# Performance work log

Hardware: AMD Instinct MI355X
Metric: run time of the kernel (lower is better)

The kernel has to match this reference:

```python
import jax, jax.numpy as jnp
import numpy as np

K = 3    # kernel_size
PAD = 1  # floor(K/2) * padding_flag


def ste_sign(x):
    # Binarize to {-1, 0, +1} (torch.sign semantics) with straight-through
    # gradient (identity), matching BNN training where grads flow to weight.org.
    return x + jax.lax.stop_gradient(jnp.sign(x) - x)


def setup_inputs() -> dict:
    key = jax.random.key(0)
    k1, k2 = jax.random.split(key)
    B, Ci, H, W = 16, 64, 32, 32
    Co = 64
    x = jax.random.normal(k1, (B, Ci, H, W), dtype=jnp.float32)
    # weight layout per module: (c_out, k, k, c_in)
    weight = jax.random.normal(k2, (Co, K, K, Ci), dtype=jnp.float32)
    return {"x": x, "weight": weight}


def reference(x, weight):
    # Majority convolution (MajorityNet): binarize input and weight to +/-1,
    # form XNOR-style products over each KxK window, take the MAJORITY (sign of
    # the spatial popcount) PER input channel, then sum majorities over input
    # channels. This is NOT a plain sum-of-products conv.
    B, Ci, H, W = x.shape
    Co = weight.shape[0]

    xb = ste_sign(x)                      # [B,Ci,H,W]  (input.size(1)!=3 -> binarized)
    wb = ste_sign(weight)                 # [Co,K,K,Ci]

    xp = jnp.pad(xb, ((0, 0), (0, 0), (PAD, PAD), (PAD, PAD)))

    # s[b,co,ci,y,x] = sum_{dy,dx} xb[b,ci,y+dy,x+dx] * wb[co,dy,dx,ci]
    s = jnp.zeros((B, Co, Ci, H, W), x.dtype)
    for dy in range(K):          # fixed K*K=9-iteration loop, fused under jit
        for dx in range(K):
            s = s + xp[:, None, :, dy:dy + H, dx:dx + W] \
                    * wb[None, :, dy, dx, :, None, None]

    # majority per input channel, then accumulate across input channels
    out = ste_sign(s).sum(axis=2)         # [B,Co,H,W]
    return out
```

## Files before the change

### kernel.cpp

```cpp
#include <hip/hip_runtime.h>
#include <stdint.h>

#define BB 16
#define CI 64
#define CO 64
#define HH 32
#define WW 32

__global__ __launch_bounds__(256) void pack_kernel(const float* __restrict__ x,
                                                   const float* __restrict__ w,
                                                   uint32_t* __restrict__ xbits,
                                                   uint32_t* __restrict__ winv) {
    const int XBLK = (BB * CI * HH * WW) / 256;
    int bid = blockIdx.x;
    if (bid < XBLK) {
        int p = bid * 256 + threadIdx.x;
        unsigned long long mask = __ballot(x[p] > 0.0f);
        int lane = threadIdx.x & 63;
        if ((lane & 31) == 0)
            xbits[p >> 5] = (lane & 32) ? (uint32_t)(mask >> 32) : (uint32_t)mask;
    } else {
        int idx = (bid - XBLK) * 256 + threadIdx.x;
        int ci = idx & 63, co = idx >> 6;
        uint32_t bits = 0;
#pragma unroll
        for (int t = 0; t < 9; ++t)
            bits |= (w[(co * 9 + t) * CI + ci] > 0.f ? 1u : 0u) << t;
        winv[ci * CO + co] = bits ^ 0x1FFu;
    }
}

__device__ __forceinline__ void fadd(uint32_t a, uint32_t b, uint32_t c,
                                     uint32_t& s, uint32_t& cy) {
    uint32_t t = a ^ b;
    s = t ^ c;
    cy = (t & c) | (a & b);
}
__device__ __forceinline__ void hadd(uint32_t a, uint32_t b, uint32_t& s, uint32_t& cy) {
    s = a ^ b;
    cy = a & b;
}
__device__ __forceinline__ void add5(const uint32_t* a, const uint32_t* b, uint32_t* r) {
    uint32_t c;
    hadd(a[0], b[0], r[0], c);
#pragma unroll
    for (int k = 1; k < 5; ++k) fadd(a[k], b[k], c, r[k], c);
    r[5] = c;
}
__device__ __forceinline__ void add6(const uint32_t* a, const uint32_t* b, uint32_t* r) {
    uint32_t c;
    hadd(a[0], b[0], r[0], c);
#pragma unroll
    for (int k = 1; k < 6; ++k) fadd(a[k], b[k], c, r[k], c);
    r[6] = c;
}

__global__ __launch_bounds__(256) void core_kernel(const uint32_t* __restrict__ xbits,
                                                   const uint32_t* __restrict__ winv,
                                                   float* __restrict__ out) {
    __shared__ uint32_t wlds[CI * CO];
    __shared__ uint4 xr4[CI];
    __shared__ uint32_t red[4][CO][5];
    __shared__ uint32_t planes7[CO][7];
    __shared__ int bord[CO][2][2];

    const int bid = blockIdx.x;
    const int tid = threadIdx.x;

    if (bid < BB * HH) {
        const int b = bid >> 5, y = bid & 31;
        if (y == 0 || y == HH - 1) return;

        {
            const uint4* src = (const uint4*)winv;
            uint4* dst = (uint4*)wlds;
#pragma unroll
            for (int i = 0; i < 4; ++i) dst[tid + i * 256] = src[tid + i * 256];
        }
        if (tid < 3 * CI) {
            int r = tid >> 6, ci = tid & 63;
            ((uint32_t*)&xr4[ci])[r] = xbits[(b * CI + ci) * HH + (y - 1 + r)];
        }
        __syncthreads();

        const int co = tid & 63, ciq = tid >> 6;

        uint32_t maj[16];
#pragma unroll
        for (int i = 0; i < 16; ++i) {
            const int ci = ciq * 16 + i;
            const uint4 xr = xr4[ci];
            const uint32_t wn = wlds[ci * CO + co];
            const uint32_t T0 = xr.x << 1, T1 = xr.x, T2 = xr.x >> 1;
            const uint32_t T3 = xr.y << 1, T4 = xr.y, T5 = xr.y >> 1;
            const uint32_t T6 = xr.z << 1, T7 = xr.z, T8 = xr.z >> 1;
            const uint32_t m0 = T0 ^ (uint32_t)(-(int)((wn >> 0) & 1));
            const uint32_t m1 = T1 ^ (uint32_t)(-(int)((wn >> 1) & 1));
            const uint32_t m2 = T2 ^ (uint32_t)(-(int)((wn >> 2) & 1));
            const uint32_t m3 = T3 ^ (uint32_t)(-(int)((wn >> 3) & 1));
            const uint32_t m4 = T4 ^ (uint32_t)(-(int)((wn >> 4) & 1));
            const uint32_t m5 = T5 ^ (uint32_t)(-(int)((wn >> 5) & 1));
            const uint32_t m6 = T6 ^ (uint32_t)(-(int)((wn >> 6) & 1));
            const uint32_t m7 = T7 ^ (uint32_t)(-(int)((wn >> 7) & 1));
            const uint32_t m8 = T8 ^ (uint32_t)(-(int)((wn >> 8) & 1));
            uint32_t s1, c1, s2, c2, s3, c3, S, C, D, E;
            fadd(m0, m1, m2, s1, c1);
            fadd(m3, m4, m5, s2, c2);
            fadd(m6, m7, m8, s3, c3);
            fadd(s1, s2, s3, S, C);
            fadd(c1, c2, c3, D, E);
            maj[i] = (E & (S | C | D)) | (~E & (S & C & D));
        }

        uint32_t A[5], Bw[5];
        fadd(maj[0], maj[1], maj[2], A[0], Bw[0]);
        fadd(maj[3], maj[4], maj[5], A[1], Bw[1]);
        fadd(maj[6], maj[7], maj[8], A[2], Bw[2]);
        fadd(maj[9], maj[10], maj[11], A[3], Bw[3]);
        fadd(maj[12], maj[13], maj[14], A[4], Bw[4]);
        uint32_t u1, v1, u2, v2, p0, v3;
        fadd(A[0], A[1], A[2], u1, v1);
        fadd(A[3], A[4], maj[15], u2, v2);
        hadd(u1, u2, p0, v3);
        uint32_t e1, f1, e2, f2, e3, f3, p1, f4;
        fadd(Bw[0], Bw[1], Bw[2], e1, f1);
        fadd(Bw[3], Bw[4], v1, e2, f2);
        fadd(e1, e2, v2, e3, f3);
        hadd(e3, v3, p1, f4);
        uint32_t g1, h1, p2, h2, p3, p4;
        fadd(f1, f2, f3, g1, h1);
        hadd(g1, f4, p2, h2);
        hadd(h1, h2, p3, p4);
        red[ciq][co][0] = p0; red[ciq][co][1] = p1; red[ciq][co][2] = p2;
        red[ciq][co][3] = p3; red[ciq][co][4] = p4;

        {
            const int fco = tid & 63, side = (tid >> 6) & 1, cih = tid >> 7;
            const int px = side * (WW - 1);
            const uint32_t rowm = (px > 0 ? 1u : 0u) | 2u | (px < WW - 1 ? 4u : 0u);
            const uint32_t vmask = rowm | (rowm << 3) | (rowm << 6);
            const uint32_t nt1 = __popc(vmask) >> 1, nt2 = (__popc(vmask) - 1) >> 1;
            uint32_t lut = 0;
            for (uint32_t m = 1; m <= 9; ++m)
                lut |= (uint32_t)((m > nt1) + (m > nt2)) << (2 * m);
            int acc = 0;
            for (int i = 0; i < 32; ++i) {
                const int ci = cih * 32 + i;
                const uint4 xr = xr4[ci];
                const uint32_t wn = wlds[ci * CO + fco];
                const uint32_t n0 = (uint32_t)((((uint64_t)xr.x) << 1) >> px) & 7u;
                const uint32_t n1 = (uint32_t)((((uint64_t)xr.y) << 1) >> px) & 7u;
                const uint32_t n2 = (uint32_t)((((uint64_t)xr.z) << 1) >> px) & 7u;
                const uint32_t xn = n0 | (n1 << 3) | (n2 << 6);
                const uint32_t mm = (uint32_t)__popc((xn ^ wn) & vmask);
                acc += (lut >> (2 * mm)) & 3u;
            }
            bord[fco][side][cih] = acc;
        }
        __syncthreads();

        if (tid < 64) {
            uint32_t x0[6], x1[6], rr[7];
            add5(red[0][tid], red[1][tid], x0);
            add5(red[2][tid], red[3][tid], x1);
            add6(x0, x1, rr);
#pragma unroll
            for (int k = 0; k < 7; ++k) planes7[tid][k] = rr[k];
        }
        __syncthreads();

        {
            const int oco = tid & 63, q = tid >> 6;
            uint32_t pl[7];
#pragma unroll
            for (int k = 0; k < 7; ++k) pl[k] = planes7[oco][k];
            float vals[8];
#pragma unroll
            for (int j = 0; j < 8; ++j) {
                const int px = q * 8 + j;
                uint32_t cnt = 0;
#pragma unroll
                for (int k = 0; k < 7; ++k) cnt += ((pl[k] >> px) & 1u) << k;
                vals[j] = (float)(2 * (int)cnt - CI);
            }
            if (q == 0) vals[0] = (float)(bord[oco][0][0] + bord[oco][0][1] - CI);
            if (q == 3) vals[7] = (float)(bord[oco][1][0] + bord[oco][1][1] - CI);
            float4* op = (float4*)&out[((size_t)(b * CO + oco) * HH + y) * WW + q * 8];
            op[0] = make_float4(vals[0], vals[1], vals[2], vals[3]);
            op[1] = make_float4(vals[4], vals[5], vals[6], vals[7]);
        }
    } else {
        const int idx = bid - BB * HH;
        const int b = idx >> 3, yb = (idx >> 2) & 1, coq = idx & 3;
        const int y = yb * (HH - 1);
        for (int i = tid; i < CI * 16; i += 256) {
            int ci = i >> 4, c = i & 15;
            wlds[i] = winv[ci * CO + coq * 16 + c];
        }
        if (tid < 3 * CI) {
            int r = tid >> 6, ci = tid & 63;
            int yy = y - 1 + r;
            ((uint32_t*)&xr4[ci])[r] = (yy >= 0 && yy < HH) ? xbits[(b * CI + ci) * HH + yy] : 0u;
        }
        __syncthreads();

        const int px = tid & 31, cog = tid >> 5;
        const uint32_t rowm = (px > 0 ? 1u : 0u) | 2u | (px < WW - 1 ? 4u : 0u);
        const uint32_t vmask = (y > 0 ? rowm : 0u) | (rowm << 3) |
                               (y < HH - 1 ? (rowm << 6) : 0u);
        const uint32_t N = __popc(vmask);
        const uint32_t nt1 = N >> 1, nt2 = (N - 1) >> 1;
        uint32_t lut = 0;
        for (uint32_t m = 1; m <= 9; ++m)
            lut |= (uint32_t)((m > nt1) + (m > nt2)) << (2 * m);
        int a0 = 0, a1 = 0;
        for (int ci = 0; ci < CI; ++ci) {
            const uint4 xr = xr4[ci];
            const uint32_t n0 = (uint32_t)((((uint64_t)xr.x) << 1) >> px) & 7u;
            const uint32_t n1 = (uint32_t)((((uint64_t)xr.y) << 1) >> px) & 7u;
            const uint32_t n2 = (uint32_t)((((uint64_t)xr.z) << 1) >> px) & 7u;
            const uint32_t xn = n0 | (n1 << 3) | (n2 << 6);
            const uint32_t w0 = wlds[ci * 16 + cog * 2 + 0];
            const uint32_t w1 = wlds[ci * 16 + cog * 2 + 1];
            uint32_t mm;
            mm = (uint32_t)__popc((xn ^ w0) & vmask); a0 += (lut >> (2 * mm)) & 3u;
            mm = (uint32_t)__popc((xn ^ w1) & vmask); a1 += (lut >> (2 * mm)) & 3u;
        }
        const int co0 = coq * 16 + cog * 2;
        out[((size_t)(b * CO + co0 + 0) * HH + y) * WW + px] = (float)(a0 - CI);
        out[((size_t)(b * CO + co0 + 1) * HH + y) * WW + px] = (float)(a1 - CI);
    }
}

extern "C" void kernel_launch(void* const* d_in, const int* in_sizes, int n_in,
                              void* d_out, int out_size, void* d_ws, size_t ws_size,
                              hipStream_t stream) {
    const float* x = (const float*)d_in[0];
    const float* w = (const float*)d_in[1];
    float* out = (float*)d_out;

    uint32_t* xbits = (uint32_t*)d_ws;
    uint32_t* winv = xbits + BB * CI * HH;

    const int XBLK = (BB * CI * HH * WW) / 256;
    pack_kernel<<<XBLK + 16, 256, 0, stream>>>(x, w, xbits, winv);
    core_kernel<<<BB * HH + 128, 256, 0, stream>>>(xbits, winv, out);
}
```

Before: 21.92 us.

## Fuse sign-packing into the core kernel and drop the separate pack launch

Removes the pack kernel and the workspace round trip: each block now binarizes its own three input rows with wave ballots and packs all 64x64 weight sign masks straight from the float weights into LDS. This saves one kernel launch and the global write and read of packed bits. In exchange every block redoes the weight packing (about 147 KB of float reads per block, mostly from cache) and reads three float rows per channel, so per-block prologue work grows considerably.

```diff
diff --git a/kernel.cpp b/kernel.cpp
--- a/kernel.cpp
+++ b/kernel.cpp
@@ -7,29 +7,6 @@
 #define HH 32
 #define WW 32
 
-__global__ __launch_bounds__(256) void pack_kernel(const float* __restrict__ x,
-                                                   const float* __restrict__ w,
-                                                   uint32_t* __restrict__ xbits,
-                                                   uint32_t* __restrict__ winv) {
-    const int XBLK = (BB * CI * HH * WW) / 256;
-    int bid = blockIdx.x;
-    if (bid < XBLK) {
-        int p = bid * 256 + threadIdx.x;
-        unsigned long long mask = __ballot(x[p] > 0.0f);
-        int lane = threadIdx.x & 63;
-        if ((lane & 31) == 0)
-            xbits[p >> 5] = (lane & 32) ? (uint32_t)(mask >> 32) : (uint32_t)mask;
-    } else {
-        int idx = (bid - XBLK) * 256 + threadIdx.x;
-        int ci = idx & 63, co = idx >> 6;
-        uint32_t bits = 0;
-#pragma unroll
-        for (int t = 0; t < 9; ++t)
-            bits |= (w[(co * 9 + t) * CI + ci] > 0.f ? 1u : 0u) << t;
-        winv[ci * CO + co] = bits ^ 0x1FFu;
-    }
-}
-
 __device__ __forceinline__ void fadd(uint32_t a, uint32_t b, uint32_t c,
                                      uint32_t& s, uint32_t& cy) {
     uint32_t t = a ^ b;
@@ -55,9 +32,9 @@
     r[6] = c;
 }
 
-__global__ __launch_bounds__(256) void core_kernel(const uint32_t* __restrict__ xbits,
-                                                   const uint32_t* __restrict__ winv,
-                                                   float* __restrict__ out) {
+__global__ __launch_bounds__(256) void fused_kernel(const float* __restrict__ x,
+                                                    const float* __restrict__ w,
+                                                    float* __restrict__ out) {
     __shared__ uint32_t wlds[CI * CO];
     __shared__ uint4 xr4[CI];
     __shared__ uint32_t red[4][CO][5];
@@ -71,15 +48,38 @@
         const int b = bid >> 5, y = bid & 31;
         if (y == 0 || y == HH - 1) return;
 
-        {
-            const uint4* src = (const uint4*)winv;
-            uint4* dst = (uint4*)wlds;
-#pragma unroll
-            for (int i = 0; i < 4; ++i) dst[tid + i * 256] = src[tid + i * 256];
-        }
-        if (tid < 3 * CI) {
-            int r = tid >> 6, ci = tid & 63;
-            ((uint32_t*)&xr4[ci])[r] = xbits[(b * CI + ci) * HH + (y - 1 + r)];
+        for (int q = tid; q < (CI / 4) * CO; q += 256) {
+            int co = q >> 4;
+            int ci0 = (q & 15) * 4;
+            uint32_t b0 = 0, b1 = 0, b2 = 0, b3 = 0;
+#pragma unroll
+            for (int t = 0; t < 9; ++t) {
+                const float4 v = *(const float4*)&w[(co * 9 + t) * CI + ci0];
+                b0 |= (v.x > 0.f ? 1u : 0u) << t;
+                b1 |= (v.y > 0.f ? 1u : 0u) << t;
+                b2 |= (v.z > 0.f ? 1u : 0u) << t;
+                b3 |= (v.w > 0.f ? 1u : 0u) << t;
+            }
+            wlds[(ci0 + 0) * CO + co] = b0 ^ 0x1FFu;
+            wlds[(ci0 + 1) * CO + co] = b1 ^ 0x1FFu;
+            wlds[(ci0 + 2) * CO + co] = b2 ^ 0x1FFu;
+            wlds[(ci0 + 3) * CO + co] = b3 ^ 0x1FFu;
+        }
+        {
+            const int wave = tid >> 6;
+            const int lane = tid & 63;
+            const int half = lane >> 5;
+            const int px = lane & 31;
+#pragma unroll
+            for (int j = 0; j < 24; ++j) {
+                int task = wave * 48 + j * 2 + half;
+                int r = task >> 6;
+                int ci = task & 63;
+                float v = x[((b * CI + ci) * HH + (y - 1 + r)) * WW + px];
+                unsigned long long mask = __ballot(v > 0.f);
+                if (px == 0)
+                    ((uint32_t*)&xr4[ci])[r] = (uint32_t)(half ? (mask >> 32) : mask);
+            }
         }
         __syncthreads();
 
@@ -139,7 +139,8 @@
             const int px = side * (WW - 1);
             const uint32_t rowm = (px > 0 ? 1u : 0u) | 2u | (px < WW - 1 ? 4u : 0u);
             const uint32_t vmask = rowm | (rowm << 3) | (rowm << 6);
-            const uint32_t nt1 = __popc(vmask) >> 1, nt2 = (__popc(vmask) - 1) >> 1;
+            const uint32_t N = __popc(vmask);
+            const uint32_t nt1 = N >> 1, nt2 = (N - 1) >> 1;
             uint32_t lut = 0;
             for (uint32_t m = 1; m <= 9; ++m)
                 lut |= (uint32_t)((m > nt1) + (m > nt2)) << (2 * m);
@@ -193,14 +194,31 @@
         const int idx = bid - BB * HH;
         const int b = idx >> 3, yb = (idx >> 2) & 1, coq = idx & 3;
         const int y = yb * (HH - 1);
-        for (int i = tid; i < CI * 16; i += 256) {
-            int ci = i >> 4, c = i & 15;
-            wlds[i] = winv[ci * CO + coq * 16 + c];
-        }
-        if (tid < 3 * CI) {
-            int r = tid >> 6, ci = tid & 63;
-            int yy = y - 1 + r;
-            ((uint32_t*)&xr4[ci])[r] = (yy >= 0 && yy < HH) ? xbits[(b * CI + ci) * HH + yy] : 0u;
+        for (int e = tid; e < CI * 16; e += 256) {
+            int ci = e >> 4, c = e & 15;
+            int co = coq * 16 + c;
+            uint32_t bits = 0;
+#pragma unroll
+            for (int t = 0; t < 9; ++t)
+                bits |= (w[(co * 9 + t) * CI + ci] > 0.f ? 1u : 0u) << t;
+            wlds[e] = bits ^ 0x1FFu;
+        }
+        {
+            const int wave = tid >> 6;
+            const int lane = tid & 63;
+            const int half = lane >> 5;
+            const int px = lane & 31;
+#pragma unroll
+            for (int j = 0; j < 24; ++j) {
+                int task = wave * 48 + j * 2 + half;
+                int r = task >> 6;
+                int ci = task & 63;
+                int yy = y - 1 + r;
+                float v = (yy >= 0 && yy < HH) ? x[((b * CI + ci) * HH + yy) * WW + px] : 0.f;
+                unsigned long long mask = __ballot(v > 0.f);
+                if (px == 0)
+                    ((uint32_t*)&xr4[ci])[r] = (uint32_t)(half ? (mask >> 32) : mask);
+            }
         }
         __syncthreads();
 
@@ -239,10 +257,5 @@
     const float* w = (const float*)d_in[1];
     float* out = (float*)d_out;
 
-    uint32_t* xbits = (uint32_t*)d_ws;
-    uint32_t* winv = xbits + BB * CI * HH;
-
-    const int XBLK = (BB * CI * HH * WW) / 256;
-    pack_kernel<<<XBLK + 16, 256, 0, stream>>>(x, w, xbits, winv);
-    core_kernel<<<BB * HH + 128, 256, 0, stream>>>(xbits, winv, out);
-}
+    fused_kernel<<<BB * HH + 128, 256, 0, stream>>>(x, w, out);
+}
```

Result: slower. 25.60 us (+16.8%).
